# Performance work log

Hardware: AMD Instinct MI355X
Metric: run time of the kernel (lower is better)

Reference implementation:

```python
import jax, jax.numpy as jnp
import numpy as np

NUM_INPUT = 700
NUM_HIDDEN = 256
NUM_OUTPUT = 20
WIN = 50
BATCH = 512
DELAYS = (0, 16, 32)
MAX_D = 32
N_LAYERS = 2
THRESH = 0.3
ALPHA = 0.8  # membrane decay tau_m
LENS = 0.5   # surrogate-gradient window

@jax.custom_vjp
def spike_fn(u):
    # Heaviside with rectangular surrogate gradient (ActFun in the torch repo)
    return (u > 0.0).astype(u.dtype)

def _spike_fwd(u):
    return spike_fn(u), u

def _spike_bwd(u, g):
    return (g * (jnp.abs(u) < LENS).astype(u.dtype),)

spike_fn.defvjp(_spike_fwd, _spike_bwd)


def setup_inputs() -> dict:
    key = jax.random.key(0)
    ks = jax.random.split(key, 6)
    def init(k, shape, fan_in):
        return (jax.random.normal(k, shape, jnp.float32) / np.sqrt(fan_in)).astype(jnp.float32)
    return {
        "x":  jax.random.uniform(ks[0], (BATCH, WIN, NUM_INPUT), jnp.float32),
        # one input Linear per delay: [n_delays, H, In]
        "Wd": init(ks[1], (len(DELAYS), NUM_HIDDEN, NUM_INPUT), NUM_INPUT),
        "bd": jnp.zeros((len(DELAYS), NUM_HIDDEN), jnp.float32),
        # per-layer feedforward and recurrent weights
        "Wf": init(ks[2], (N_LAYERS, NUM_HIDDEN, NUM_HIDDEN), NUM_HIDDEN),
        "bf": jnp.zeros((N_LAYERS, NUM_HIDDEN), jnp.float32),
        "Wr": init(ks[3], (N_LAYERS, NUM_HIDDEN, NUM_HIDDEN), NUM_HIDDEN),
        # readout
        "Wo": init(ks[4], (NUM_OUTPUT, NUM_HIDDEN), NUM_HIDDEN),
        "bo": jnp.zeros((NUM_OUTPUT,), jnp.float32),
    }


def _forward(x, Wd, bd, Wf, bf, Wr, Wo, bo):
    B, win, _ = x.shape
    # extended_input: zeros for the first MAX_D steps, then the input
    ext = jnp.pad(x, ((0, 0), (MAX_D, 0), (0, 0)))
    # Precompute summed delayed input currents for all timesteps at once.
    cur = jnp.zeros((B, win, NUM_HIDDEN), x.dtype)
    for i, d in enumerate(DELAYS):
        sl = jax.lax.dynamic_slice_in_dim(ext, MAX_D - d, win, axis=1)
        cur = cur + jnp.einsum('bti,hi->bth', sl, Wd[i]) + bd[i]

    def step(carry, cur_t):
        mems, spks, o_mem, o_spk, o_sum, out_mot = carry
        prev = cur_t  # [B, H] summed delayed-input activations
        new_m, new_s = [], []
        for l in range(N_LAYERS):
            m = mems[l] * ALPHA * (1.0 - spks[l]) + prev @ Wf[l].T + bf[l] + spks[l] @ Wr[l].T
            s = spike_fn(m - THRESH)
            new_m.append(m)
            new_s.append(s)
            prev = s
        o_mem = o_mem * ALPHA * (1.0 - o_spk) + prev @ Wo.T + bo
        o_spk = spike_fn(o_mem - THRESH)
        o_sum = o_sum + o_spk
        out_mot = out_mot + jax.nn.softmax(o_mem, axis=1)
        return (jnp.stack(new_m), jnp.stack(new_s), o_mem, o_spk, o_sum, out_mot), None

    z = jnp.zeros((B, NUM_OUTPUT), x.dtype)
    zh = jnp.zeros((N_LAYERS, B, NUM_HIDDEN), x.dtype)
    carry0 = (zh, zh, z, z, z, z)
    carry, _ = jax.lax.scan(step, carry0, jnp.swapaxes(cur, 0, 1))
    _, _, _, _, o_sum, out_mot = carry
    return (o_sum / win, out_mot)


def reference(x, Wd, bd, Wf, bf, Wr, Wo, bo):
    return _forward(x, Wd, bd, Wf, bf, Wr, Wo, bo)
```

## Files before the change

### kernel.cpp

```cpp
#include <hip/hip_runtime.h>
#include <cstddef>

#define CUR_ELEMS (25600 * 256)
#define WROWS 65792

__global__ __launch_bounds__(256) void k0_transpose(
    const float* __restrict__ Wf, const float* __restrict__ Wr,
    const float* __restrict__ Wo, float* __restrict__ ws) {
  int tid = blockIdx.x * blockDim.x + threadIdx.x;
  float* Wr0T = ws + CUR_ELEMS;
  float* Wf1T = Wr0T + WROWS;
  float* Wr1T = Wf1T + WROWS;
  float* WoT  = Wr1T + WROWS;
  if (tid < WROWS) {
    int k = tid >> 8, h = tid & 255;
    Wr0T[tid] = (k < 256) ? Wr[h * 256 + k] : 0.f;
  } else if (tid < 2 * WROWS) {
    int i = tid - WROWS; int k = i >> 8, h = i & 255;
    Wf1T[i] = (k < 256) ? Wf[65536 + h * 256 + k] : 0.f;
  } else if (tid < 3 * WROWS) {
    int i = tid - 2 * WROWS; int k = i >> 8, h = i & 255;
    Wr1T[i] = (k < 256) ? Wr[65536 + h * 256 + k] : 0.f;
  } else if (tid < 3 * WROWS + 5140) {
    int i = tid - 3 * WROWS; int k = i / 20, j = i - k * 20;
    WoT[i] = (k < 256) ? Wo[j * 256 + k] : 0.f;
  }
}

__global__ __launch_bounds__(256) void k1_cur(
    const float* __restrict__ x, const float* __restrict__ Wd,
    const float* __restrict__ bd, float* __restrict__ cur) {
  __shared__ float As[16][132];
  __shared__ float Bs[16][132];
  const int t  = 49 - blockIdx.y;
  const int bt = blockIdx.x >> 1, ht = blockIdx.x & 1;
  const int b0 = bt * 128, h0 = ht * 128;
  const int tid = threadIdx.x;
  const int tx = tid & 15, ty = tid >> 4;
  const int r = tid & 127, half = tid >> 7;
  const int kk0a = half * 8;

  float acc[8][8];
#pragma unroll
  for (int i = 0; i < 8; ++i)
#pragma unroll
    for (int j = 0; j < 8; ++j) acc[i][j] = 0.f;

  const int DEL[3] = {0, 16, 32};
#pragma unroll 1
  for (int di = 0; di < 3; ++di) {
    const int d = DEL[di];
    if (t < d) continue;
    const int tsrc = t - d;
    const float* Arow = x + ((size_t)(b0 + r) * 50 + tsrc) * 700;
    const float* Brow = Wd + (size_t)di * 179200 + (size_t)(h0 + r) * 700;
    float4 pa0, pa1, pb0, pb1;
    {
      pa0 = *(const float4*)(Arow + kk0a);
      pa1 = *(const float4*)(Arow + kk0a + 4);
      pb0 = *(const float4*)(Brow + kk0a);
      pb1 = *(const float4*)(Brow + kk0a + 4);
    }
#pragma unroll 1
    for (int c = 0; c < 44; ++c) {
      __syncthreads();
      As[kk0a + 0][r] = pa0.x; As[kk0a + 1][r] = pa0.y;
      As[kk0a + 2][r] = pa0.z; As[kk0a + 3][r] = pa0.w;
      As[kk0a + 4][r] = pa1.x; As[kk0a + 5][r] = pa1.y;
      As[kk0a + 6][r] = pa1.z; As[kk0a + 7][r] = pa1.w;
      Bs[kk0a + 0][r] = pb0.x; Bs[kk0a + 1][r] = pb0.y;
      Bs[kk0a + 2][r] = pb0.z; Bs[kk0a + 3][r] = pb0.w;
      Bs[kk0a + 4][r] = pb1.x; Bs[kk0a + 5][r] = pb1.y;
      Bs[kk0a + 6][r] = pb1.z; Bs[kk0a + 7][r] = pb1.w;
      __syncthreads();
      if (c + 1 < 44) {
        const int i0 = (c + 1) * 16 + kk0a, i1 = i0 + 4;
        pa0 = (i0 < 700) ? *(const float4*)(Arow + i0)
                         : make_float4(0.f, 0.f, 0.f, 0.f);
        pa1 = (i1 < 700) ? *(const float4*)(Arow + i1)
                         : make_float4(0.f, 0.f, 0.f, 0.f);
        pb0 = (i0 < 700) ? *(const float4*)(Brow + i0)
                         : make_float4(0.f, 0.f, 0.f, 0.f);
        pb1 = (i1 < 700) ? *(const float4*)(Brow + i1)
                         : make_float4(0.f, 0.f, 0.f, 0.f);
      }
#pragma unroll
      for (int kk = 0; kk < 16; ++kk) {
        const float4 a0 = *(const float4*)&As[kk][ty * 4];
        const float4 a1 = *(const float4*)&As[kk][64 + ty * 4];
        const float4 c0 = *(const float4*)&Bs[kk][tx * 4];
        const float4 c1 = *(const float4*)&Bs[kk][64 + tx * 4];
        const float ar[8] = {a0.x, a0.y, a0.z, a0.w, a1.x, a1.y, a1.z, a1.w};
        const float br[8] = {c0.x, c0.y, c0.z, c0.w, c1.x, c1.y, c1.z, c1.w};
#pragma unroll
        for (int rr = 0; rr < 8; ++rr)
#pragma unroll
          for (int cc = 0; cc < 8; ++cc) acc[rr][cc] += ar[rr] * br[cc];
      }
    }
  }
  float bias[8];
#pragma unroll
  for (int q = 0; q < 2; ++q)
#pragma unroll
    for (int c = 0; c < 4; ++c) {
      const int col = h0 + q * 64 + tx * 4 + c;
      bias[q * 4 + c] = bd[col] + bd[256 + col] + bd[512 + col];
    }
#pragma unroll
  for (int p = 0; p < 2; ++p)
#pragma unroll
    for (int rr = 0; rr < 4; ++rr) {
      const int row = b0 + p * 64 + ty * 4 + rr;
      float* dst = cur + ((size_t)t * 512 + row) * 256 + h0;
      const int ai = p * 4 + rr;
      float4 v0 = make_float4(acc[ai][0] + bias[0], acc[ai][1] + bias[1],
                              acc[ai][2] + bias[2], acc[ai][3] + bias[3]);
      float4 v1 = make_float4(acc[ai][4] + bias[4], acc[ai][5] + bias[5],
                              acc[ai][6] + bias[6], acc[ai][7] + bias[7]);
      *(float4*)(dst + tx * 4) = v0;
      *(float4*)(dst + 64 + tx * 4) = v1;
    }
}

__global__ __launch_bounds__(256) void k1b_ff0(
    const float* __restrict__ Wf, const float* __restrict__ bf,
    float* __restrict__ cur) {
  __shared__ float As[16][68];
  __shared__ float Bs[16][260];
  const int m0 = blockIdx.x * 64;
  const int tid = threadIdx.x;
  const int tx = tid & 15, ty = tid >> 4;
  const int lr = tid & 63, akk = (tid >> 6) * 4;

  float acc[4][16];
#pragma unroll
  for (int i = 0; i < 4; ++i)
#pragma unroll
    for (int j = 0; j < 16; ++j) acc[i][j] = 0.f;

#pragma unroll 1
  for (int k0 = 0; k0 < 256; k0 += 16) {
    float4 av = *(const float4*)(cur + (size_t)(m0 + lr) * 256 + k0 + akk);
    As[akk + 0][lr] = av.x; As[akk + 1][lr] = av.y;
    As[akk + 2][lr] = av.z; As[akk + 3][lr] = av.w;
#pragma unroll
    for (int e = 0; e < 4; ++e) {
      const int hh = e * 64 + lr;
      float4 bv = *(const float4*)(Wf + (size_t)hh * 256 + k0 + akk);
      Bs[akk + 0][hh] = bv.x; Bs[akk + 1][hh] = bv.y;
      Bs[akk + 2][hh] = bv.z; Bs[akk + 3][hh] = bv.w;
    }
    __syncthreads();
#pragma unroll
    for (int kk = 0; kk < 16; ++kk) {
      const float4 a = *(const float4*)&As[kk][ty * 4];
      const float ar[4] = {a.x, a.y, a.z, a.w};
#pragma unroll
      for (int q = 0; q < 4; ++q) {
        const float4 bq = *(const float4*)&Bs[kk][q * 64 + tx * 4];
        const float br[4] = {bq.x, bq.y, bq.z, bq.w};
#pragma unroll
        for (int rr = 0; rr < 4; ++rr)
#pragma unroll
          for (int cc = 0; cc < 4; ++cc)
            acc[rr][q * 4 + cc] += ar[rr] * br[cc];
      }
    }
    __syncthreads();
  }
  float bias[16];
#pragma unroll
  for (int q = 0; q < 4; ++q)
#pragma unroll
    for (int c = 0; c < 4; ++c) bias[q * 4 + c] = bf[q * 64 + tx * 4 + c];
#pragma unroll
  for (int rr = 0; rr < 4; ++rr) {
    float* dst = cur + (size_t)(m0 + ty * 4 + rr) * 256;
#pragma unroll
    for (int q = 0; q < 4; ++q) {
      float4 v = make_float4(acc[rr][q * 4 + 0] + bias[q * 4 + 0],
                             acc[rr][q * 4 + 1] + bias[q * 4 + 1],
                             acc[rr][q * 4 + 2] + bias[q * 4 + 2],
                             acc[rr][q * 4 + 3] + bias[q * 4 + 3]);
      *(float4*)(dst + q * 64 + tx * 4) = v;
    }
  }
}

__device__ __forceinline__ void load8rows(const float* __restrict__ W,
                                          const int* LC, int j, int l4,
                                          float4* w) {
  const int4 a = *(const int4*)(LC + j);
  const int4 c = *(const int4*)(LC + j + 4);
  w[0] = *(const float4*)(W + a.x + l4);
  w[1] = *(const float4*)(W + a.y + l4);
  w[2] = *(const float4*)(W + a.z + l4);
  w[3] = *(const float4*)(W + a.w + l4);
  w[4] = *(const float4*)(W + c.x + l4);
  w[5] = *(const float4*)(W + c.y + l4);
  w[6] = *(const float4*)(W + c.z + l4);
  w[7] = *(const float4*)(W + c.w + l4);
}

__device__ __forceinline__ void add8rows(float4& acc, const float4* w) {
  float4 t0, t1, t2, t3;
  t0.x = w[0].x + w[1].x; t0.y = w[0].y + w[1].y; t0.z = w[0].z + w[1].z; t0.w = w[0].w + w[1].w;
  t1.x = w[2].x + w[3].x; t1.y = w[2].y + w[3].y; t1.z = w[2].z + w[3].z; t1.w = w[2].w + w[3].w;
  t2.x = w[4].x + w[5].x; t2.y = w[4].y + w[5].y; t2.z = w[4].z + w[5].z; t2.w = w[4].w + w[5].w;
  t3.x = w[6].x + w[7].x; t3.y = w[6].y + w[7].y; t3.z = w[6].z + w[7].z; t3.w = w[6].w + w[7].w;
  t0.x += t1.x; t0.y += t1.y; t0.z += t1.z; t0.w += t1.w;
  t2.x += t3.x; t2.y += t3.y; t2.z += t3.z; t2.w += t3.w;
  acc.x += t0.x + t2.x; acc.y += t0.y + t2.y;
  acc.z += t0.z + t2.z; acc.w += t0.w + t2.w;
}

__device__ __forceinline__ float4 gather_rows(const float* __restrict__ W,
                                              const int* LC, int n, int l4) {
  float4 acc = make_float4(0.f, 0.f, 0.f, 0.f);
  const int G = n >> 3;
  if (G == 0) return acc;
  float4 wa[8], wb[8];
  load8rows(W, LC, 0, l4, wa);
  int g = 1;
  for (; g + 2 <= G; g += 2) {
    load8rows(W, LC, g * 8, l4, wb);
    add8rows(acc, wa);
    load8rows(W, LC, (g + 1) * 8, l4, wa);
    add8rows(acc, wb);
  }
  if (g < G) {
    load8rows(W, LC, g * 8, l4, wb);
    add8rows(acc, wa);
    add8rows(acc, wb);
  } else {
    add8rows(acc, wa);
  }
  return acc;
}

__device__ __forceinline__ void load8o(const float* __restrict__ W,
                                       const int* LCb, int j, int lane,
                                       float* w) {
  const int4 a = *(const int4*)(LCb + j);
  const int4 c = *(const int4*)(LCb + j + 4);
  w[0] = W[a.x + lane]; w[1] = W[a.y + lane];
  w[2] = W[a.z + lane]; w[3] = W[a.w + lane];
  w[4] = W[c.x + lane]; w[5] = W[c.y + lane];
  w[6] = W[c.z + lane]; w[7] = W[c.w + lane];
}

__device__ __forceinline__ float add8o(const float* w) {
  return ((w[0] + w[1]) + (w[2] + w[3])) + ((w[4] + w[5]) + (w[6] + w[7]));
}

__device__ __forceinline__ float gather_out(const float* __restrict__ W,
                                            const int* LCb, int n, int lane) {
  float acc = 0.f;
  const int G = n >> 3;
  if (G == 0) return acc;
  float wa[8], wb[8];
  load8o(W, LCb, 0, lane, wa);
  int g = 1;
  for (; g + 2 <= G; g += 2) {
    load8o(W, LCb, g * 8, lane, wb);
    acc += add8o(wa);
    load8o(W, LCb, (g + 1) * 8, lane, wa);
    acc += add8o(wb);
  }
  if (g < G) {
    load8o(W, LCb, g * 8, lane, wb);
    acc += add8o(wa);
    acc += add8o(wb);
  } else {
    acc += add8o(wa);
  }
  return acc;
}

__global__ __launch_bounds__(64) void k2_scan(
    const float* __restrict__ ff0, const float* __restrict__ Wr0T,
    const float* __restrict__ Wf1T, const float* __restrict__ Wr1T,
    const float* __restrict__ WoT, const float* __restrict__ bf,
    const float* __restrict__ bo, float* __restrict__ out) {
  __shared__ __align__(16) int LC0[264];
  __shared__ __align__(16) int LC1[264];
  __shared__ __align__(16) int LCb[264];
  __shared__ float obuf[20];
  const int b = blockIdx.x;
  const int lane = threadIdx.x;
  const int l4 = lane * 4;
  const unsigned long long lb = (1ull << lane) - 1ull;

  float4 m0 = make_float4(0.f, 0.f, 0.f, 0.f), m1 = m0;
  float4 s0v = m0, s1v = m0;
  const float4 bf1v = *(const float4*)(bf + 256 + l4);
  float omem = 0.f, ospk = 0.f, osum = 0.f, omot = 0.f;
  const float bov = (lane < 20) ? bo[lane] : 0.f;
  int n0 = 0, n1 = 0;

  const float* ffp = ff0 + (size_t)b * 256 + l4;
  float4 ff = *(const float4*)ffp;

#pragma unroll 1
  for (int t = 0; t < 50; ++t) {
    float4 ffn = ff;
    if (t < 49) ffn = *(const float4*)(ffp + (size_t)(t + 1) * 131072);
    {
      const float4 g = gather_rows(Wr0T, LC0, n0, l4);
      m0.x = m0.x * 0.8f * (1.f - s0v.x) + ff.x + g.x;
      m0.y = m0.y * 0.8f * (1.f - s0v.y) + ff.y + g.y;
      m0.z = m0.z * 0.8f * (1.f - s0v.z) + ff.z + g.z;
      m0.w = m0.w * 0.8f * (1.f - s0v.w) + ff.w + g.w;
      s0v.x = (m0.x - 0.3f > 0.f) ? 1.f : 0.f;
      s0v.y = (m0.y - 0.3f > 0.f) ? 1.f : 0.f;
      s0v.z = (m0.z - 0.3f > 0.f) ? 1.f : 0.f;
      s0v.w = (m0.w - 0.3f > 0.f) ? 1.f : 0.f;
    }
    {
      const float sv[4] = {s0v.x, s0v.y, s0v.z, s0v.w};
      int base = 0;
#pragma unroll
      for (int q = 0; q < 4; ++q) {
        const bool sp = sv[q] > 0.f;
        const unsigned long long mk = __ballot(sp);
        const int pos = base + (int)__popcll(mk & lb);
        if (sp) LC0[pos] = (l4 + q) << 8;
        base += (int)__popcll(mk);
      }
      const int pad = (-base) & 7;
      if (lane < pad) LC0[base + lane] = 256 << 8;
      n0 = base + pad;
    }
    {
      const float4 g1 = gather_rows(Wf1T, LC0, n0, l4);
      const float4 g2 = gather_rows(Wr1T, LC1, n1, l4);
      m1.x = m1.x * 0.8f * (1.f - s1v.x) + bf1v.x + g1.x + g2.x;
      m1.y = m1.y * 0.8f * (1.f - s1v.y) + bf1v.y + g1.y + g2.y;
      m1.z = m1.z * 0.8f * (1.f - s1v.z) + bf1v.z + g1.z + g2.z;
      m1.w = m1.w * 0.8f * (1.f - s1v.w) + bf1v.w + g1.w + g2.w;
      s1v.x = (m1.x - 0.3f > 0.f) ? 1.f : 0.f;
      s1v.y = (m1.y - 0.3f > 0.f) ? 1.f : 0.f;
      s1v.z = (m1.z - 0.3f > 0.f) ? 1.f : 0.f;
      s1v.w = (m1.w - 0.3f > 0.f) ? 1.f : 0.f;
    }
    {
      const float sv[4] = {s1v.x, s1v.y, s1v.z, s1v.w};
      int base = 0;
#pragma unroll
      for (int q = 0; q < 4; ++q) {
        const bool sp = sv[q] > 0.f;
        const unsigned long long mk = __ballot(sp);
        const int pos = base + (int)__popcll(mk & lb);
        if (sp) { LC1[pos] = (l4 + q) << 8; LCb[pos] = (l4 + q) * 20; }
        base += (int)__popcll(mk);
      }
      const int pad = (-base) & 7;
      if (lane < pad) { LC1[base + lane] = 256 << 8; LCb[base + lane] = 256 * 20; }
      n1 = base + pad;
    }
    if (lane < 20) {
      const float v = gather_out(WoT, LCb, n1, lane);
      omem = omem * 0.8f * (1.f - ospk) + bov + v;
      ospk = (omem - 0.3f > 0.f) ? 1.f : 0.f;
      osum += ospk;
      obuf[lane] = omem;
    }
    if (lane < 20) {
      float ov[20];
#pragma unroll
      for (int j = 0; j < 20; ++j) ov[j] = obuf[j];
      float mx = ov[0];
#pragma unroll
      for (int j = 1; j < 20; ++j) mx = fmaxf(mx, ov[j]);
      float sm = 0.f;
#pragma unroll
      for (int j = 0; j < 20; ++j) sm += expf(ov[j] - mx);
      omot += expf(omem - mx) / sm;
    }
    ff = ffn;
  }
  if (lane < 20) {
    out[b * 20 + lane] = osum / 50.0f;
    out[10240 + b * 20 + lane] = omot;
  }
}

extern "C" void kernel_launch(void* const* d_in, const int* in_sizes, int n_in,
                              void* d_out, int out_size, void* d_ws, size_t ws_size,
                              hipStream_t stream) {
  const float* x  = (const float*)d_in[0];
  const float* Wd = (const float*)d_in[1];
  const float* bd = (const float*)d_in[2];
  const float* Wf = (const float*)d_in[3];
  const float* bf = (const float*)d_in[4];
  const float* Wr = (const float*)d_in[5];
  const float* Wo = (const float*)d_in[6];
  const float* bo = (const float*)d_in[7];
  float* out = (float*)d_out;
  float* ws  = (float*)d_ws;

  float* cur  = ws;
  float* Wr0T = ws + CUR_ELEMS;
  float* Wf1T = Wr0T + WROWS;
  float* Wr1T = Wf1T + WROWS;
  float* WoT  = Wr1T + WROWS;

  hipLaunchKernelGGL(k0_transpose, dim3(792), dim3(256), 0, stream, Wf, Wr, Wo, ws);
  hipLaunchKernelGGL(k1_cur, dim3(8, 50), dim3(256), 0, stream, x, Wd, bd, cur);
  hipLaunchKernelGGL(k1b_ff0, dim3(400), dim3(256), 0, stream, Wf, bf, cur);
  hipLaunchKernelGGL(k2_scan, dim3(512), dim3(64), 0, stream, cur, Wr0T, Wf1T,
                     Wr1T, WoT, bf, bo, out);
}
```

Baseline: 940.6 us.

## Double-buffer GEMM tiles, deepen gather prefetch, and parallelize readout from LDS

The input-current GEMM kernel now double-buffers its shared-memory A/B tiles. This replaces the two barriers per k-chunk with one and overlaps tile stores with compute. In the scan kernel, the sparse row gather keeps four groups of eight rows in flight, so spike lists are padded to multiples of 32. The readout weights are staged in LDS and the output projection is split across 60 lanes (three per output) with a shuffle reduction, instead of 20 lanes walking every spike. The cost is more LDS and registers, plus extra padded dummy rows gathered per step.

Measured after the change: 890.5 us. 5.3% less time.

```diff
diff --git a/kernel.cpp b/kernel.cpp
--- a/kernel.cpp
+++ b/kernel.cpp
@@ -30,8 +30,8 @@
 __global__ __launch_bounds__(256) void k1_cur(
     const float* __restrict__ x, const float* __restrict__ Wd,
     const float* __restrict__ bd, float* __restrict__ cur) {
-  __shared__ float As[16][132];
-  __shared__ float Bs[16][132];
+  __shared__ float As[2][16][132];
+  __shared__ float Bs[2][16][132];
   const int t  = 49 - blockIdx.y;
   const int bt = blockIdx.x >> 1, ht = blockIdx.x & 1;
   const int b0 = bt * 128, h0 = ht * 128;
@@ -55,41 +55,53 @@
     const float* Arow = x + ((size_t)(b0 + r) * 50 + tsrc) * 700;
     const float* Brow = Wd + (size_t)di * 179200 + (size_t)(h0 + r) * 700;
     float4 pa0, pa1, pb0, pb1;
-    {
-      pa0 = *(const float4*)(Arow + kk0a);
-      pa1 = *(const float4*)(Arow + kk0a + 4);
-      pb0 = *(const float4*)(Brow + kk0a);
-      pb1 = *(const float4*)(Brow + kk0a + 4);
-    }
+    pa0 = *(const float4*)(Arow + kk0a);
+    pa1 = *(const float4*)(Arow + kk0a + 4);
+    pb0 = *(const float4*)(Brow + kk0a);
+    pb1 = *(const float4*)(Brow + kk0a + 4);
+    As[0][kk0a + 0][r] = pa0.x; As[0][kk0a + 1][r] = pa0.y;
+    As[0][kk0a + 2][r] = pa0.z; As[0][kk0a + 3][r] = pa0.w;
+    As[0][kk0a + 4][r] = pa1.x; As[0][kk0a + 5][r] = pa1.y;
+    As[0][kk0a + 6][r] = pa1.z; As[0][kk0a + 7][r] = pa1.w;
+    Bs[0][kk0a + 0][r] = pb0.x; Bs[0][kk0a + 1][r] = pb0.y;
+    Bs[0][kk0a + 2][r] = pb0.z; Bs[0][kk0a + 3][r] = pb0.w;
+    Bs[0][kk0a + 4][r] = pb1.x; Bs[0][kk0a + 5][r] = pb1.y;
+    Bs[0][kk0a + 6][r] = pb1.z; Bs[0][kk0a + 7][r] = pb1.w;
+    pa0 = *(const float4*)(Arow + 16 + kk0a);
+    pa1 = *(const float4*)(Arow + 16 + kk0a + 4);
+    pb0 = *(const float4*)(Brow + 16 + kk0a);
+    pb1 = *(const float4*)(Brow + 16 + kk0a + 4);
+    __syncthreads();
 #pragma unroll 1
     for (int c = 0; c < 44; ++c) {
-      __syncthreads();
-      As[kk0a + 0][r] = pa0.x; As[kk0a + 1][r] = pa0.y;
-      As[kk0a + 2][r] = pa0.z; As[kk0a + 3][r] = pa0.w;
-      As[kk0a + 4][r] = pa1.x; As[kk0a + 5][r] = pa1.y;
-      As[kk0a + 6][r] = pa1.z; As[kk0a + 7][r] = pa1.w;
-      Bs[kk0a + 0][r] = pb0.x; Bs[kk0a + 1][r] = pb0.y;
-      Bs[kk0a + 2][r] = pb0.z; Bs[kk0a + 3][r] = pb0.w;
-      Bs[kk0a + 4][r] = pb1.x; Bs[kk0a + 5][r] = pb1.y;
-      Bs[kk0a + 6][r] = pb1.z; Bs[kk0a + 7][r] = pb1.w;
-      __syncthreads();
-      if (c + 1 < 44) {
-        const int i0 = (c + 1) * 16 + kk0a, i1 = i0 + 4;
-        pa0 = (i0 < 700) ? *(const float4*)(Arow + i0)
-                         : make_float4(0.f, 0.f, 0.f, 0.f);
-        pa1 = (i1 < 700) ? *(const float4*)(Arow + i1)
-                         : make_float4(0.f, 0.f, 0.f, 0.f);
-        pb0 = (i0 < 700) ? *(const float4*)(Brow + i0)
-                         : make_float4(0.f, 0.f, 0.f, 0.f);
-        pb1 = (i1 < 700) ? *(const float4*)(Brow + i1)
-                         : make_float4(0.f, 0.f, 0.f, 0.f);
+      const int cb = c & 1, nb = cb ^ 1;
+      if (c < 43) {
+        As[nb][kk0a + 0][r] = pa0.x; As[nb][kk0a + 1][r] = pa0.y;
+        As[nb][kk0a + 2][r] = pa0.z; As[nb][kk0a + 3][r] = pa0.w;
+        As[nb][kk0a + 4][r] = pa1.x; As[nb][kk0a + 5][r] = pa1.y;
+        As[nb][kk0a + 6][r] = pa1.z; As[nb][kk0a + 7][r] = pa1.w;
+        Bs[nb][kk0a + 0][r] = pb0.x; Bs[nb][kk0a + 1][r] = pb0.y;
+        Bs[nb][kk0a + 2][r] = pb0.z; Bs[nb][kk0a + 3][r] = pb0.w;
+        Bs[nb][kk0a + 4][r] = pb1.x; Bs[nb][kk0a + 5][r] = pb1.y;
+        Bs[nb][kk0a + 6][r] = pb1.z; Bs[nb][kk0a + 7][r] = pb1.w;
+      }
+      if (c < 42) {
+        const int i0 = (c + 2) * 16 + kk0a, i1 = i0 + 4;
+        pa0 = (i0 + 3 < 700) ? *(const float4*)(Arow + i0)
+                             : make_float4(0.f, 0.f, 0.f, 0.f);
+        pa1 = (i1 + 3 < 700) ? *(const float4*)(Arow + i1)
+                             : make_float4(0.f, 0.f, 0.f, 0.f);
+        pb0 = (i0 + 3 < 700) ? *(const float4*)(Brow + i0)
+                             : make_float4(0.f, 0.f, 0.f, 0.f);
+        pb1 = (i1 + 3 < 700) ? *(const float4*)(Brow + i1)
+                             : make_float4(0.f, 0.f, 0.f, 0.f);
       }
 #pragma unroll
       for (int kk = 0; kk < 16; ++kk) {
-        const float4 a0 = *(const float4*)&As[kk][ty * 4];
-        const float4 a1 = *(const float4*)&As[kk][64 + ty * 4];
-        const float4 c0 = *(const float4*)&Bs[kk][tx * 4];
-        const float4 c1 = *(const float4*)&Bs[kk][64 + tx * 4];
+        const float4 a0 = *(const float4*)&As[cb][kk][ty * 4];
+        const float4 a1 = *(const float4*)&As[cb][kk][64 + ty * 4];
+        const float4 c0 = *(const float4*)&Bs[cb][kk][tx * 4];
+        const float4 c1 = *(const float4*)&Bs[cb][kk][64 + tx * 4];
         const float ar[8] = {a0.x, a0.y, a0.z, a0.w, a1.x, a1.y, a1.z, a1.w};
         const float br[8] = {c0.x, c0.y, c0.z, c0.w, c1.x, c1.y, c1.z, c1.w};
 #pragma unroll
@@ -97,6 +109,7 @@
 #pragma unroll
           for (int cc = 0; cc < 8; ++cc) acc[rr][cc] += ar[rr] * br[cc];
       }
+      __syncthreads();
     }
   }
   float bias[8];
@@ -220,62 +233,25 @@
   float4 acc = make_float4(0.f, 0.f, 0.f, 0.f);
   const int G = n >> 3;
   if (G == 0) return acc;
-  float4 wa[8], wb[8];
-  load8rows(W, LC, 0, l4, wa);
-  int g = 1;
-  for (; g + 2 <= G; g += 2) {
-    load8rows(W, LC, g * 8, l4, wb);
-    add8rows(acc, wa);
-    load8rows(W, LC, (g + 1) * 8, l4, wa);
-    add8rows(acc, wb);
-  }
-  if (g < G) {
-    load8rows(W, LC, g * 8, l4, wb);
-    add8rows(acc, wa);
-    add8rows(acc, wb);
-  } else {
-    add8rows(acc, wa);
-  }
+  float4 w0[8], w1[8], w2[8], w3[8];
+  load8rows(W, LC, 0,  l4, w0);
+  load8rows(W, LC, 8,  l4, w1);
+  load8rows(W, LC, 16, l4, w2);
+  load8rows(W, LC, 24, l4, w3);
+  int g = 4;
+  for (; g + 4 <= G; g += 4) {
+    add8rows(acc, w0); load8rows(W, LC, (g + 0) * 8, l4, w0);
+    add8rows(acc, w1); load8rows(W, LC, (g + 1) * 8, l4, w1);
+    add8rows(acc, w2); load8rows(W, LC, (g + 2) * 8, l4, w2);
+    add8rows(acc, w3); load8rows(W, LC, (g + 3) * 8, l4, w3);
+  }
+  add8rows(acc, w0); add8rows(acc, w1);
+  add8rows(acc, w2); add8rows(acc, w3);
   return acc;
-}
-
-__device__ __forceinline__ void load8o(const float* __restrict__ W,
-                                       const int* LCb, int j, int lane,
-                                       float* w) {
-  const int4 a = *(const int4*)(LCb + j);
-  const int4 c = *(const int4*)(LCb + j + 4);
-  w[0] = W[a.x + lane]; w[1] = W[a.y + lane];
-  w[2] = W[a.z + lane]; w[3] = W[a.w + lane];
-  w[4] = W[c.x + lane]; w[5] = W[c.y + lane];
-  w[6] = W[c.z + lane]; w[7] = W[c.w + lane];
 }
 
 __device__ __forceinline__ float add8o(const float* w) {
   return ((w[0] + w[1]) + (w[2] + w[3])) + ((w[4] + w[5]) + (w[6] + w[7]));
-}
-
-__device__ __forceinline__ float gather_out(const float* __restrict__ W,
-                                            const int* LCb, int n, int lane) {
-  float acc = 0.f;
-  const int G = n >> 3;
-  if (G == 0) return acc;
-  float wa[8], wb[8];
-  load8o(W, LCb, 0, lane, wa);
-  int g = 1;
-  for (; g + 2 <= G; g += 2) {
-    load8o(W, LCb, g * 8, lane, wb);
-    acc += add8o(wa);
-    load8o(W, LCb, (g + 1) * 8, lane, wa);
-    acc += add8o(wb);
-  }
-  if (g < G) {
-    load8o(W, LCb, g * 8, lane, wb);
-    acc += add8o(wa);
-    acc += add8o(wb);
-  } else {
-    acc += add8o(wa);
-  }
-  return acc;
 }
 
 __global__ __launch_bounds__(64) void k2_scan(
@@ -283,21 +259,26 @@
     const float* __restrict__ Wf1T, const float* __restrict__ Wr1T,
     const float* __restrict__ WoT, const float* __restrict__ bf,
     const float* __restrict__ bo, float* __restrict__ out) {
-  __shared__ __align__(16) int LC0[264];
-  __shared__ __align__(16) int LC1[264];
-  __shared__ __align__(16) int LCb[264];
+  __shared__ __align__(16) int LC0[288];
+  __shared__ __align__(16) int LC1[288];
+  __shared__ __align__(16) int LCb[280];
+  __shared__ float WoTl[5140];
   __shared__ float obuf[20];
   const int b = blockIdx.x;
   const int lane = threadIdx.x;
   const int l4 = lane * 4;
   const unsigned long long lb = (1ull << lane) - 1ull;
 
+  for (int i = lane; i < 1285; i += 64)
+    *(float4*)(WoTl + 4 * i) = *(const float4*)(WoT + 4 * i);
+
   float4 m0 = make_float4(0.f, 0.f, 0.f, 0.f), m1 = m0;
   float4 s0v = m0, s1v = m0;
   const float4 bf1v = *(const float4*)(bf + 256 + l4);
   float omem = 0.f, ospk = 0.f, osum = 0.f, omot = 0.f;
   const float bov = (lane < 20) ? bo[lane] : 0.f;
-  int n0 = 0, n1 = 0;
+  const int ro = lane / 3, rc = lane - ro * 3;
+  int n0 = 0, n1g = 0, n1r = 0;
 
   const float* ffp = ff0 + (size_t)b * 256 + l4;
   float4 ff = *(const float4*)ffp;
@@ -328,13 +309,13 @@
         if (sp) LC0[pos] = (l4 + q) << 8;
         base += (int)__popcll(mk);
       }
-      const int pad = (-base) & 7;
+      const int pad = (-base) & 31;
       if (lane < pad) LC0[base + lane] = 256 << 8;
       n0 = base + pad;
     }
     {
       const float4 g1 = gather_rows(Wf1T, LC0, n0, l4);
-      const float4 g2 = gather_rows(Wr1T, LC1, n1, l4);
+      const float4 g2 = gather_rows(Wr1T, LC1, n1g, l4);
       m1.x = m1.x * 0.8f * (1.f - s1v.x) + bf1v.x + g1.x + g2.x;
       m1.y = m1.y * 0.8f * (1.f - s1v.y) + bf1v.y + g1.y + g2.y;
       m1.z = m1.z * 0.8f * (1.f - s1v.z) + bf1v.z + g1.z + g2.z;
@@ -355,28 +336,52 @@
         if (sp) { LC1[pos] = (l4 + q) << 8; LCb[pos] = (l4 + q) * 20; }
         base += (int)__popcll(mk);
       }
-      const int pad = (-base) & 7;
-      if (lane < pad) { LC1[base + lane] = 256 << 8; LCb[base + lane] = 256 * 20; }
-      n1 = base + pad;
-    }
-    if (lane < 20) {
-      const float v = gather_out(WoT, LCb, n1, lane);
-      omem = omem * 0.8f * (1.f - ospk) + bov + v;
-      ospk = (omem - 0.3f > 0.f) ? 1.f : 0.f;
-      osum += ospk;
-      obuf[lane] = omem;
-    }
-    if (lane < 20) {
-      float ov[20];
-#pragma unroll
-      for (int j = 0; j < 20; ++j) ov[j] = obuf[j];
-      float mx = ov[0];
-#pragma unroll
-      for (int j = 1; j < 20; ++j) mx = fmaxf(mx, ov[j]);
-      float sm = 0.f;
-#pragma unroll
-      for (int j = 0; j < 20; ++j) sm += expf(ov[j] - mx);
-      omot += expf(omem - mx) / sm;
+      const int padg = (-base) & 31;
+      if (lane < padg) LC1[base + lane] = 256 << 8;
+      n1g = base + padg;
+      const int rem = base % 24;
+      const int padr = rem ? (24 - rem) : 0;
+      if (lane < padr) LCb[base + lane] = 256 * 20;
+      n1r = base + padr;
+    }
+    {
+      float v = 0.f;
+      if (lane < 60) {
+        const int GR = n1r / 24;
+        int j = rc;
+        for (int g = 0; g < GR; ++g) {
+          int idx[8]; float w[8];
+#pragma unroll
+          for (int u = 0; u < 8; ++u) idx[u] = LCb[j + 3 * u];
+#pragma unroll
+          for (int u = 0; u < 8; ++u) w[u] = WoTl[idx[u] + ro];
+          v += add8o(w);
+          j += 24;
+        }
+      }
+      const float v1 = __shfl_down(v, 1);
+      const float v2 = __shfl_down(v, 2);
+      v += v1 + v2;
+      if (rc == 0 && lane < 60) obuf[ro] = v;
+      if (lane < 20) {
+        const float oacc = bov + obuf[lane];
+        omem = omem * 0.8f * (1.f - ospk) + oacc;
+        ospk = (omem - 0.3f > 0.f) ? 1.f : 0.f;
+        osum += ospk;
+        obuf[lane] = omem;
+      }
+      if (lane < 20) {
+        float ov[20];
+#pragma unroll
+        for (int j2 = 0; j2 < 20; ++j2) ov[j2] = obuf[j2];
+        float mx = ov[0];
+#pragma unroll
+        for (int j2 = 1; j2 < 20; ++j2) mx = fmaxf(mx, ov[j2]);
+        float sm = 0.f;
+#pragma unroll
+        for (int j2 = 0; j2 < 20; ++j2) sm += expf(ov[j2] - mx);
+        omot += expf(omem - mx) / sm;
+      }
     }
     ff = ffn;
   }
```
